# Kernel tuning notes

Measured on AMD Instinct MI355X. Metric: run time of the kernel, lower is better.

Reference implementation:

```python
import jax, jax.numpy as jnp
import numpy as np

N = 50000       # num_node
E = 800000      # num edges (avg degree 32)
F_IN, F_HID, F_OUT = 128, 128, 64


def setup_inputs() -> dict:
    key = jax.random.key(0)
    ks = jax.random.split(key, 8)
    x = jax.random.normal(ks[0], (N, F_IN), dtype=jnp.float32)
    edge_index = jax.random.randint(ks[1], (2, E), 0, N, dtype=jnp.int64)
    edge_weight = jax.random.uniform(ks[2], (E,), dtype=jnp.float32)
    s1 = 1.0 / np.sqrt(F_IN)
    s2 = 1.0 / np.sqrt(F_HID)
    W1 = jax.random.normal(ks[3], (F_HID, F_IN), dtype=jnp.float32) * s1
    b1 = jnp.zeros((F_HID,), dtype=jnp.float32)
    W2 = jax.random.normal(ks[4], (F_HID, F_HID), dtype=jnp.float32) * s2
    b2 = jnp.zeros((F_HID,), dtype=jnp.float32)
    W3 = jax.random.normal(ks[5], (F_OUT, F_HID), dtype=jnp.float32) * s2
    b3 = jnp.zeros((F_OUT,), dtype=jnp.float32)
    return {"x": x, "edge_index": edge_index, "edge_weight": edge_weight,
            "W1": W1, "b1": b1, "W2": W2, "b2": b2, "W3": W3, "b3": b3}


def _gcn_norm(edge_index, edge_weight, num_nodes):
    # PyG gcn_norm: add self-loops (weight 1), symmetric D^-1/2 (A+I) D^-1/2
    loop = jnp.arange(num_nodes, dtype=edge_index.dtype)
    row = jnp.concatenate([edge_index[0], loop])  # source
    col = jnp.concatenate([edge_index[1], loop])  # target (aggregation index)
    ew = jnp.concatenate([edge_weight, jnp.ones((num_nodes,), edge_weight.dtype)])
    deg = jax.ops.segment_sum(ew, col, num_segments=num_nodes)
    deg_safe = jnp.where(deg > 0, deg, 1.0)
    dinv = jnp.where(deg > 0, jax.lax.rsqrt(deg_safe), 0.0)
    norm = dinv[row] * ew * dinv[col]  # [E+N]
    return row, col, norm


def reference(x, edge_index, edge_weight, W1, b1, W2, b2, W3, b3):
    num_nodes = x.shape[0]
    row, col, norm = _gcn_norm(edge_index, edge_weight, num_nodes)
    h = x
    for W, b in ((W1, b1), (W2, b2), (W3, b3)):
        m = h @ W.T                                   # [N, d_out]
        msg = m[row] * norm[:, None]                  # gather + scale, [E+N, d_out]
        agg = jax.ops.segment_sum(msg, col, num_segments=num_nodes)
        h = jax.nn.relu(agg + b)                      # GCNConv bias then ReLU
    return h.reshape(-1)                              # torch.flatten
```

## Files before the change

### kernel.cpp

```cpp
#include <hip/hip_runtime.h>
#include <hip/hip_fp16.h>


#define K_DIM 128
#define SORT_ITEMS 4096

typedef unsigned long long u64;
typedef unsigned int u32;

using half8   = __attribute__((ext_vector_type(8))) _Float16;
using floatx4 = __attribute__((ext_vector_type(4))) float;


__global__ void build_hist(const int* __restrict__ row, const int* __restrict__ col,
                           const float* __restrict__ ew, u64* __restrict__ el,
                           u32* __restrict__ ghist, int E, int N, int nb,
                           const float* __restrict__ W1, const float* __restrict__ W2,
                           const float* __restrict__ W3, __half* __restrict__ Wh,
                           int nw1, int nw2, int nw3) {
    const int b = blockIdx.x;
    if (b >= nb) {
        const int i = (b - nb) * 256 + threadIdx.x;
        const int tot = nw1 + nw2 + nw3;
        if (i < tot) {
            float v = (i < nw1) ? W1[i] : (i < nw1 + nw2 ? W2[i - nw1] : W3[i - nw1 - nw2]);
            Wh[i] = __float2half_rn(v);
        }
        return;
    }
    __shared__ u32 bin[256];
    bin[threadIdx.x] = 0;
    __syncthreads();
    const int total = E + N;
    const int base = b * SORT_ITEMS;
    const int end = min(base + SORT_ITEMS, total);
    for (int i = base + threadIdx.x; i < end; i += 256) {
        u64 e;
        if (i < E) {
            e = ((u64)(u32)col[i] << 48) | ((u64)(u32)row[i] << 32)
              | (u64)__float_as_uint(ew[i]);
        } else {
            int v = i - E;
            e = ((u64)(u32)v << 48) | ((u64)(u32)v << 32)
              | (u64)__float_as_uint(1.0f);
        }
        el[i] = e;
        atomicAdd(&bin[(u32)(e >> 56)], 1u);
    }
    __syncthreads();
    ghist[(size_t)threadIdx.x * nb + b] = bin[threadIdx.x];
}

__global__ void digit_sum(const u32* __restrict__ ghist, u32* __restrict__ dsum, int nb) {
    __shared__ u32 s[256];
    const int d = blockIdx.x;
    u32 acc = 0;
    for (int i = threadIdx.x; i < nb; i += 256) acc += ghist[(size_t)d * nb + i];
    s[threadIdx.x] = acc;
    __syncthreads();
    for (int off = 128; off > 0; off >>= 1) {
        if (threadIdx.x < off) s[threadIdx.x] += s[threadIdx.x + off];
        __syncthreads();
    }
    if (threadIdx.x == 0) dsum[d] = s[0];
}

__global__ void digit_scan(u32* __restrict__ ghist, const u32* __restrict__ dsum,
                           u32* __restrict__ dbase, int nb) {
    __shared__ u32 ds[256];
    __shared__ u32 s[256];
    const int d = blockIdx.x, t = threadIdx.x;
    ds[t] = dsum[t];
    __syncthreads();
    for (int off = 1; off < 256; off <<= 1) {
        u32 u = (t >= off) ? ds[t - off] : 0;
        __syncthreads();
        ds[t] += u;
        __syncthreads();
    }
    u32 carry = (d == 0) ? 0u : ds[d - 1];
    if (t == 0) dbase[d] = carry;
    if (d == 255 && t == 0) dbase[256] = ds[255];
    for (int base = 0; base < nb; base += 256) {
        const int i = base + t;
        const u32 v = (i < nb) ? ghist[(size_t)d * nb + i] : 0;
        s[t] = v;
        __syncthreads();
        for (int off = 1; off < 256; off <<= 1) {
            u32 u = (t >= off) ? s[t - off] : 0;
            __syncthreads();
            s[t] += u;
            __syncthreads();
        }
        if (i < nb) ghist[(size_t)d * nb + i] = carry + s[t] - v;
        carry += s[255];
        __syncthreads();
    }
}

__global__ __launch_bounds__(256) void p1_scatter(const u64* __restrict__ el,
                                                  const u32* __restrict__ ghist,
                                                  u64* __restrict__ out, int total, int nb) {
    __shared__ u32 gbase[256];
    __shared__ u32 lbase[256];
    __shared__ u32 lcur[256];
    __shared__ u64 buf[SORT_ITEMS];
    const int t = threadIdx.x;
    gbase[t] = ghist[(size_t)t * nb + blockIdx.x];
    lcur[t] = 0;
    __syncthreads();
    const int base = blockIdx.x * SORT_ITEMS;
    const int end = min(base + SORT_ITEMS, total);
    const int cnt = end - base;

    u64 it[16];
    bool ok[16];
#pragma unroll
    for (int j = 0; j < 16; ++j) {
        const int i = base + t + j * 256;
        ok[j] = i < end;
        it[j] = ok[j] ? el[i] : 0;
        if (ok[j]) atomicAdd(&lcur[(u32)(it[j] >> 56)], 1u);
    }
    __syncthreads();
    const u32 v = lcur[t];
    lbase[t] = v;
    __syncthreads();
    for (int off = 1; off < 256; off <<= 1) {
        u32 u = (t >= off) ? lbase[t - off] : 0;
        __syncthreads();
        lbase[t] += u;
        __syncthreads();
    }
    const u32 excl = lbase[t] - v;
    __syncthreads();
    lbase[t] = excl;
    lcur[t] = excl;
    __syncthreads();
#pragma unroll
    for (int j = 0; j < 16; ++j) {
        if (ok[j]) {
            const u32 d = (u32)(it[j] >> 56);
            const u32 p = atomicAdd(&lcur[d], 1u);
            buf[p] = it[j];
        }
    }
    __syncthreads();
    for (int i = t; i < cnt; i += 256) {
        const u64 e = buf[i];
        const u32 d = (u32)(e >> 56);
        out[gbase[d] + i - lbase[d]] = e;
    }
}

__global__ void p2_sort(const u64* __restrict__ in, u64* __restrict__ out,
                        const u32* __restrict__ dbase,
                        int* __restrict__ offs, float* __restrict__ dinv, int n) {
    const int t = threadIdx.x;
    const int base = (int)dbase[blockIdx.x];
    const int size = (int)dbase[blockIdx.x + 1] - base;
    __shared__ u32 hist[256], cur[256], s[256];
    __shared__ float wsum[256];
    hist[t] = 0;
    wsum[t] = 0.f;
    __syncthreads();
    for (int i = t; i < size; i += 256)
        atomicAdd(&hist[(u32)(in[base + i] >> 48) & 0xFFu], 1u);
    __syncthreads();
    const u32 v = hist[t];
    s[t] = v;
    __syncthreads();
    for (int off = 1; off < 256; off <<= 1) {
        u32 u = (t >= off) ? s[t - off] : 0;
        __syncthreads();
        s[t] += u;
        __syncthreads();
    }
    const u32 mystart = (u32)base + s[t] - v;
    cur[t] = mystart;
    __syncthreads();
    for (int i = t; i < size; i += 256) {
        u64 e = in[base + i];
        u32 lo = (u32)(e >> 48) & 0xFFu;
        u32 p = atomicAdd(&cur[lo], 1u);
        out[p] = e;
        atomicAdd(&wsum[lo], __uint_as_float((u32)(e & 0xFFFFFFFFu)));
    }
    __syncthreads();
    const int node = blockIdx.x * 256 + t;
    if (node < n && v > 0) {
        offs[node] = (int)mystart;
        dinv[node] = rsqrtf(wsum[t]);
        if (node == n - 1) offs[n] = (int)(mystart + v);
    }
}


template <int BN, bool FP32IN>
__global__ __launch_bounds__(256) void mfma_gemm(const void* __restrict__ Ain,
                                                 const __half* __restrict__ Wh,
                                                 const float* __restrict__ dinv,
                                                 __half* __restrict__ C, int nrows) {
    constexpr int NT = BN / 16;
    const int wave = threadIdx.x >> 6;
    const int lane = threadIdx.x & 63;
    const int quad = lane >> 4;
    const int l16  = lane & 15;
    const int row0 = blockIdx.x * 64 + wave * 16;

    int arow = row0 + l16;
    if (arow > nrows - 1) arow = nrows - 1;

    floatx4 acc[NT] = {};

#pragma unroll
    for (int kc = 0; kc < 4; ++kc) {
        const int kof = kc * 32 + quad * 8;
        half8 af;
        if constexpr (FP32IN) {
            const float* ap = (const float*)Ain + (size_t)arow * K_DIM + kof;
            float4 f0 = *(const float4*)ap;
            float4 f1 = *(const float4*)(ap + 4);
            af[0] = (_Float16)f0.x; af[1] = (_Float16)f0.y;
            af[2] = (_Float16)f0.z; af[3] = (_Float16)f0.w;
            af[4] = (_Float16)f1.x; af[5] = (_Float16)f1.y;
            af[6] = (_Float16)f1.z; af[7] = (_Float16)f1.w;
        } else {
            af = *(const half8*)((const __half*)Ain + (size_t)arow * K_DIM + kof);
        }
#pragma unroll
        for (int ct = 0; ct < NT; ++ct) {
            half8 bf = *(const half8*)(Wh + (size_t)(ct * 16 + l16) * K_DIM + kof);
            acc[ct] = __builtin_amdgcn_mfma_f32_16x16x32_f16(af, bf, acc[ct], 0, 0, 0);
        }
    }

    float dv[4];
    int grow[4];
    bool ok[4];
#pragma unroll
    for (int r = 0; r < 4; ++r) {
        grow[r] = row0 + quad * 4 + r;
        ok[r] = grow[r] < nrows;
        dv[r] = ok[r] ? dinv[grow[r]] : 0.f;
    }
#pragma unroll
    for (int ct = 0; ct < NT; ++ct) {
        const int colb = ct * 16 + l16;
#pragma unroll
        for (int r = 0; r < 4; ++r)
            if (ok[r])
                C[(size_t)grow[r] * BN + colb] = __float2half_rn(acc[ct][r] * dv[r]);
    }
}


template <int D, typename OUT>
__global__ __launch_bounds__(256) void agg_kernel(
    const __half* __restrict__ m, const int* __restrict__ offs,
    const int2* __restrict__ csr, const float* __restrict__ dinv,
    const float* __restrict__ bias, OUT* __restrict__ out, int n) {
    const int wid = threadIdx.x >> 6;
    const int lane = threadIdx.x & 63;
    const int node = (blockIdx.x << 2) + wid;
    if (node >= n) return;
    const int beg = offs[node];
    const int end = offs[node + 1];
    const int cnt = end - beg;
    const int rem = cnt & 7;
    const __half2* mh = (const __half2*)m;
    float acc0 = 0.f, acc1 = 0.f;

    if constexpr (D == 128) {
        int k = beg;
        if (rem) {
            int2 e[8];
            float2 f[8];
#pragma unroll
            for (int j = 0; j < 8; ++j) e[j] = csr[k + (j < rem ? j : 0)];
#pragma unroll
            for (int j = 0; j < 8; ++j)
                f[j] = __half22float2(mh[(size_t)(e[j].y & 0xFFFF) * 64 + lane]);
#pragma unroll
            for (int j = 0; j < 8; ++j) {
                float w = (j < rem) ? __int_as_float(e[j].x) : 0.f;
                acc0 = fmaf(w, f[j].x, acc0);
                acc1 = fmaf(w, f[j].y, acc1);
            }
            k += rem;
        }
        for (; k < end; k += 8) {
            int2 e[8];
            float2 f[8];
#pragma unroll
            for (int j = 0; j < 8; ++j) e[j] = csr[k + j];
#pragma unroll
            for (int j = 0; j < 8; ++j)
                f[j] = __half22float2(mh[(size_t)(e[j].y & 0xFFFF) * 64 + lane]);
#pragma unroll
            for (int j = 0; j < 8; ++j) {
                float w = __int_as_float(e[j].x);
                acc0 = fmaf(w, f[j].x, acc0);
                acc1 = fmaf(w, f[j].y, acc1);
            }
        }
        const float dv = dinv[node];
        const float2 bv = *(const float2*)(bias + 2 * lane);
        float ox = fmaxf(acc0 * dv + bv.x, 0.f);
        float oy = fmaxf(acc1 * dv + bv.y, 0.f);
        if constexpr (sizeof(OUT) == 2) {
            ((__half2*)out)[(size_t)node * 64 + lane] = __floats2half2_rn(ox, oy);
        } else {
            *(float2*)((float*)out + (size_t)node * 128 + 2 * lane) = make_float2(ox, oy);
        }
    } else {
        const int half = lane >> 5;
        const int sl = lane & 31;
        int k = beg;
        if (rem) {
            int2 e[4];
            float2 f[4];
#pragma unroll
            for (int jj = 0; jj < 4; ++jj) {
                const int idx = 2 * jj + half;
                e[jj] = csr[k + (idx < rem ? idx : 0)];
            }
#pragma unroll
            for (int jj = 0; jj < 4; ++jj)
                f[jj] = __half22float2(mh[(size_t)(e[jj].y & 0xFFFF) * 32 + sl]);
#pragma unroll
            for (int jj = 0; jj < 4; ++jj) {
                const int idx = 2 * jj + half;
                float w = (idx < rem) ? __int_as_float(e[jj].x) : 0.f;
                acc0 = fmaf(w, f[jj].x, acc0);
                acc1 = fmaf(w, f[jj].y, acc1);
            }
            k += rem;
        }
        for (; k < end; k += 8) {
            int2 e0 = csr[k + half], e1 = csr[k + 2 + half];
            int2 e2 = csr[k + 4 + half], e3 = csr[k + 6 + half];
            float2 f0 = __half22float2(mh[(size_t)(e0.y & 0xFFFF) * 32 + sl]);
            float2 f1 = __half22float2(mh[(size_t)(e1.y & 0xFFFF) * 32 + sl]);
            float2 f2 = __half22float2(mh[(size_t)(e2.y & 0xFFFF) * 32 + sl]);
            float2 f3 = __half22float2(mh[(size_t)(e3.y & 0xFFFF) * 32 + sl]);
            float w0 = __int_as_float(e0.x), w1 = __int_as_float(e1.x);
            float w2 = __int_as_float(e2.x), w3 = __int_as_float(e3.x);
            acc0 = fmaf(w0, f0.x, acc0); acc1 = fmaf(w0, f0.y, acc1);
            acc0 = fmaf(w1, f1.x, acc0); acc1 = fmaf(w1, f1.y, acc1);
            acc0 = fmaf(w2, f2.x, acc0); acc1 = fmaf(w2, f2.y, acc1);
            acc0 = fmaf(w3, f3.x, acc0); acc1 = fmaf(w3, f3.y, acc1);
        }
        acc0 += __shfl_xor(acc0, 32);
        acc1 += __shfl_xor(acc1, 32);
        if (half == 0) {
            const float dv = dinv[node];
            const float2 bv = *(const float2*)(bias + 2 * sl);
            float ox = fmaxf(acc0 * dv + bv.x, 0.f);
            float oy = fmaxf(acc1 * dv + bv.y, 0.f);
            *(float2*)((float*)out + (size_t)node * 64 + 2 * sl) = make_float2(ox, oy);
        }
    }
}


extern "C" void kernel_launch(void* const* d_in, const int* in_sizes, int n_in,
                              void* d_out, int out_size, void* d_ws, size_t ws_size,
                              hipStream_t stream) {
    const float* x  = (const float*)d_in[0];
    const int*   ei = (const int*)d_in[1];
    const float* ew = (const float*)d_in[2];
    const float* W1 = (const float*)d_in[3];
    const float* b1 = (const float*)d_in[4];
    const float* W2 = (const float*)d_in[5];
    const float* b2 = (const float*)d_in[6];
    const float* W3 = (const float*)d_in[7];
    const float* b3 = (const float*)d_in[8];
    float* out = (float*)d_out;

    const int N = in_sizes[0] / K_DIM;
    const int E = in_sizes[2];
    const int* row = ei;
    const int* col = ei + E;

    const int total = E + N;
    const int nb = (total + SORT_ITEMS - 1) / SORT_ITEMS;
    const int ngroups = (N + 255) >> 8;
    const int NW1 = 128 * 128, NW2 = 128 * 128, NW3 = 64 * 128;
    const int nwb = (NW1 + NW2 + NW3 + 255) / 256;

    u64* elA      = (u64*)d_ws;
    u64* elB      = elA + total;
    __half* m_buf = (__half*)(elB + total);
    __half* h_buf = m_buf + (size_t)N * K_DIM;
    __half* Wh    = h_buf + (size_t)N * K_DIM;
    u32* ghist    = (u32*)(Wh + NW1 + NW2 + NW3);
    u32* dsum     = ghist + (size_t)256 * nb;
    u32* dbase    = dsum + 256;
    int* offs     = (int*)(dbase + 257);
    float* dinv   = (float*)(offs + N + 1);

    build_hist<<<nb + nwb, 256, 0, stream>>>(row, col, ew, elA, ghist, E, N, nb,
                                             W1, W2, W3, Wh, NW1, NW2, NW3);
    digit_sum<<<256, 256, 0, stream>>>(ghist, dsum, nb);
    digit_scan<<<256, 256, 0, stream>>>(ghist, dsum, dbase, nb);
    p1_scatter<<<nb, 256, 0, stream>>>(elA, ghist, elB, total, nb);
    p2_sort<<<ngroups, 256, 0, stream>>>(elB, elA, dbase, offs, dinv, N);

    const int gemm_blocks = (N + 63) / 64;
    const int agg_blocks = (N + 3) / 4;
    const int2* csr = (const int2*)elA;

    mfma_gemm<128, true><<<gemm_blocks, 256, 0, stream>>>(x, Wh, dinv, m_buf, N);
    agg_kernel<128, __half><<<agg_blocks, 256, 0, stream>>>(m_buf, offs, csr, dinv, b1, h_buf, N);
    mfma_gemm<128, false><<<gemm_blocks, 256, 0, stream>>>(h_buf, Wh + NW1, dinv, m_buf, N);
    agg_kernel<128, __half><<<agg_blocks, 256, 0, stream>>>(m_buf, offs, csr, dinv, b2, h_buf, N);
    mfma_gemm<64, false><<<gemm_blocks, 256, 0, stream>>>(h_buf, Wh + NW1 + NW2, dinv, m_buf, N);
    agg_kernel<64, float><<<agg_blocks, 256, 0, stream>>>(m_buf, offs, csr, dinv, b3, out, N);
}
```

Before: 288.3 us.

## Rework GCN aggregation to wave-cooperative edge loads and 16-byte feature gathers

The aggregation kernel now loads up to 64 CSR entries per node in one coalesced wave load and broadcasts weight and source index with shuffles, instead of each lane reading edges serially. Each gather is a 16-byte half8 load per lane, so several edges are processed at once by lane groups. Partial sums are combined with xor-shuffle reductions before bias, ReLU and store. The intent is fewer, wider memory transactions and more gathers in flight per wave, at the cost of extra shuffle reductions and of dropping the float-output branch for D=128.

```diff
diff --git a/kernel.cpp b/kernel.cpp
--- a/kernel.cpp
+++ b/kernel.cpp
@@ -267,98 +267,99 @@
     const int beg = offs[node];
     const int end = offs[node + 1];
     const int cnt = end - beg;
-    const int rem = cnt & 7;
-    const __half2* mh = (const __half2*)m;
-    float acc0 = 0.f, acc1 = 0.f;
+    const half8* mrow = (const half8*)m;
+
+    const int2 ev = csr[beg + min(lane, cnt - 1)];
+    const float wv = (lane < cnt) ? __int_as_float(ev.x) : 0.f;
+    const int   sv = ev.y & 0xFFFF;
+    const int nr = min(cnt, 64);
+
+    float acc[8] = {0.f, 0.f, 0.f, 0.f, 0.f, 0.f, 0.f, 0.f};
 
     if constexpr (D == 128) {
-        int k = beg;
-        if (rem) {
-            int2 e[8];
-            float2 f[8];
-#pragma unroll
-            for (int j = 0; j < 8; ++j) e[j] = csr[k + (j < rem ? j : 0)];
-#pragma unroll
-            for (int j = 0; j < 8; ++j)
-                f[j] = __half22float2(mh[(size_t)(e[j].y & 0xFFFF) * 64 + lane]);
-#pragma unroll
-            for (int j = 0; j < 8; ++j) {
-                float w = (j < rem) ? __int_as_float(e[j].x) : 0.f;
-                acc0 = fmaf(w, f[j].x, acc0);
-                acc1 = fmaf(w, f[j].y, acc1);
-            }
-            k += rem;
-        }
-        for (; k < end; k += 8) {
-            int2 e[8];
-            float2 f[8];
-#pragma unroll
-            for (int j = 0; j < 8; ++j) e[j] = csr[k + j];
-#pragma unroll
-            for (int j = 0; j < 8; ++j)
-                f[j] = __half22float2(mh[(size_t)(e[j].y & 0xFFFF) * 64 + lane]);
-#pragma unroll
-            for (int j = 0; j < 8; ++j) {
-                float w = __int_as_float(e[j].x);
-                acc0 = fmaf(w, f[j].x, acc0);
-                acc1 = fmaf(w, f[j].y, acc1);
-            }
-        }
-        const float dv = dinv[node];
-        const float2 bv = *(const float2*)(bias + 2 * lane);
-        float ox = fmaxf(acc0 * dv + bv.x, 0.f);
-        float oy = fmaxf(acc1 * dv + bv.y, 0.f);
-        if constexpr (sizeof(OUT) == 2) {
-            ((__half2*)out)[(size_t)node * 64 + lane] = __floats2half2_rn(ox, oy);
-        } else {
-            *(float2*)((float*)out + (size_t)node * 128 + 2 * lane) = make_float2(ox, oy);
+        const int quad = lane >> 4;
+        const int l16  = lane & 15;
+        for (int r = 0; r * 4 < nr; ++r) {
+            const int j = r * 4 + quad;
+            const bool ok = j < nr;
+            float w = __shfl(wv, j);
+            int   s = __shfl(sv, j);
+            w = ok ? w : 0.f;
+            s = ok ? s : 0;
+            half8 hv = mrow[(size_t)s * 16 + l16];
+#pragma unroll
+            for (int i = 0; i < 8; ++i)
+                acc[i] = fmaf(w, (float)hv[i], acc[i]);
+        }
+        for (int k = beg + 64 + quad; k < end; k += 4) {
+            const int2 e0 = csr[k];
+            const float w0 = __int_as_float(e0.x);
+            half8 hv = mrow[(size_t)(e0.y & 0xFFFF) * 16 + l16];
+#pragma unroll
+            for (int i = 0; i < 8; ++i)
+                acc[i] = fmaf(w0, (float)hv[i], acc[i]);
+        }
+#pragma unroll
+        for (int i = 0; i < 8; ++i) {
+            acc[i] += __shfl_xor(acc[i], 16);
+            acc[i] += __shfl_xor(acc[i], 32);
+        }
+        if (quad == 0) {
+            const float dv = dinv[node];
+            const float4 b0 = *(const float4*)(bias + l16 * 8);
+            const float4 b1 = *(const float4*)(bias + l16 * 8 + 4);
+            const float bb[8] = {b0.x, b0.y, b0.z, b0.w, b1.x, b1.y, b1.z, b1.w};
+            half8 ho;
+#pragma unroll
+            for (int i = 0; i < 8; ++i)
+                ho[i] = (_Float16)fmaxf(acc[i] * dv + bb[i], 0.f);
+            *(half8*)((__half*)out + (size_t)node * 128 + l16 * 8) = ho;
         }
     } else {
-        const int half = lane >> 5;
-        const int sl = lane & 31;
-        int k = beg;
-        if (rem) {
-            int2 e[4];
-            float2 f[4];
-#pragma unroll
-            for (int jj = 0; jj < 4; ++jj) {
-                const int idx = 2 * jj + half;
-                e[jj] = csr[k + (idx < rem ? idx : 0)];
-            }
-#pragma unroll
-            for (int jj = 0; jj < 4; ++jj)
-                f[jj] = __half22float2(mh[(size_t)(e[jj].y & 0xFFFF) * 32 + sl]);
-#pragma unroll
-            for (int jj = 0; jj < 4; ++jj) {
-                const int idx = 2 * jj + half;
-                float w = (idx < rem) ? __int_as_float(e[jj].x) : 0.f;
-                acc0 = fmaf(w, f[jj].x, acc0);
-                acc1 = fmaf(w, f[jj].y, acc1);
-            }
-            k += rem;
-        }
-        for (; k < end; k += 8) {
-            int2 e0 = csr[k + half], e1 = csr[k + 2 + half];
-            int2 e2 = csr[k + 4 + half], e3 = csr[k + 6 + half];
-            float2 f0 = __half22float2(mh[(size_t)(e0.y & 0xFFFF) * 32 + sl]);
-            float2 f1 = __half22float2(mh[(size_t)(e1.y & 0xFFFF) * 32 + sl]);
-            float2 f2 = __half22float2(mh[(size_t)(e2.y & 0xFFFF) * 32 + sl]);
-            float2 f3 = __half22float2(mh[(size_t)(e3.y & 0xFFFF) * 32 + sl]);
-            float w0 = __int_as_float(e0.x), w1 = __int_as_float(e1.x);
-            float w2 = __int_as_float(e2.x), w3 = __int_as_float(e3.x);
-            acc0 = fmaf(w0, f0.x, acc0); acc1 = fmaf(w0, f0.y, acc1);
-            acc0 = fmaf(w1, f1.x, acc0); acc1 = fmaf(w1, f1.y, acc1);
-            acc0 = fmaf(w2, f2.x, acc0); acc1 = fmaf(w2, f2.y, acc1);
-            acc0 = fmaf(w3, f3.x, acc0); acc1 = fmaf(w3, f3.y, acc1);
-        }
-        acc0 += __shfl_xor(acc0, 32);
-        acc1 += __shfl_xor(acc1, 32);
-        if (half == 0) {
+        const int oct = lane >> 3;
+        const int l8  = lane & 7;
+        for (int r = 0; r * 8 < nr; ++r) {
+            const int j = r * 8 + oct;
+            const bool ok = j < nr;
+            float w = __shfl(wv, j);
+            int   s = __shfl(sv, j);
+            w = ok ? w : 0.f;
+            s = ok ? s : 0;
+            half8 hv = mrow[(size_t)s * 8 + l8];
+#pragma unroll
+            for (int i = 0; i < 8; ++i)
+                acc[i] = fmaf(w, (float)hv[i], acc[i]);
+        }
+        for (int k = beg + 64 + oct; k < end; k += 8) {
+            const int2 e0 = csr[k];
+            const float w0 = __int_as_float(e0.x);
+            half8 hv = mrow[(size_t)(e0.y & 0xFFFF) * 8 + l8];
+#pragma unroll
+            for (int i = 0; i < 8; ++i)
+                acc[i] = fmaf(w0, (float)hv[i], acc[i]);
+        }
+#pragma unroll
+        for (int i = 0; i < 8; ++i) {
+            acc[i] += __shfl_xor(acc[i], 8);
+            acc[i] += __shfl_xor(acc[i], 16);
+            acc[i] += __shfl_xor(acc[i], 32);
+        }
+        if (oct == 0) {
             const float dv = dinv[node];
-            const float2 bv = *(const float2*)(bias + 2 * sl);
-            float ox = fmaxf(acc0 * dv + bv.x, 0.f);
-            float oy = fmaxf(acc1 * dv + bv.y, 0.f);
-            *(float2*)((float*)out + (size_t)node * 64 + 2 * sl) = make_float2(ox, oy);
+            const float4 b0 = *(const float4*)(bias + l8 * 8);
+            const float4 b1 = *(const float4*)(bias + l8 * 8 + 4);
+            float4 v0, v1;
+            v0.x = fmaxf(acc[0] * dv + b0.x, 0.f);
+            v0.y = fmaxf(acc[1] * dv + b0.y, 0.f);
+            v0.z = fmaxf(acc[2] * dv + b0.z, 0.f);
+            v0.w = fmaxf(acc[3] * dv + b0.w, 0.f);
+            v1.x = fmaxf(acc[4] * dv + b1.x, 0.f);
+            v1.y = fmaxf(acc[5] * dv + b1.y, 0.f);
+            v1.z = fmaxf(acc[6] * dv + b1.z, 0.f);
+            v1.w = fmaxf(acc[7] * dv + b1.w, 0.f);
+            float* op = (float*)out + (size_t)node * 64 + l8 * 8;
+            *(float4*)op = v0;
+            *(float4*)(op + 4) = v1;
         }
     }
 }
```

Result: faster. 282.1 us (-2.2%).
